# Optimization experiments

Measured on AMD Instinct MI355X. Metric: run time of the kernel, lower is better.

Reference implementation:

```python
import jax, jax.numpy as jnp
import numpy as np

EPS = 1e-5

def _layer_norm_last(x):
    # F.layer_norm over the last dim, no affine
    m = jnp.mean(x, axis=-1, keepdims=True)
    v = jnp.var(x, axis=-1, keepdims=True)
    return (x - m) * jax.lax.rsqrt(v + EPS)

def setup_inputs() -> dict:
    key = jax.random.key(0)
    ks = jax.random.split(key, 4)
    N, C, H, W = 8, 512, 32, 32
    G = 8
    x = jax.random.normal(ks[0], (N, C, H, W), dtype=jnp.float32)
    w_qkv = jax.random.normal(ks[1], (3 * C, C), dtype=jnp.float32) * 0.02
    relative = jax.random.normal(ks[2], (3, 2 * C - 1), dtype=jnp.float32)
    bn_w = jnp.ones((3 * G,), dtype=jnp.float32)
    bn_b = jnp.zeros((3 * G,), dtype=jnp.float32)
    return {
        "x": x, "w_qkv": w_qkv, "relative": relative,
        "bn_w": bn_w, "bn_b": bn_b,
        "f_qr": jnp.float32(0.1), "f_kr": jnp.float32(0.1),
        "f_sv": jnp.float32(1.0), "f_sve": jnp.float32(0.1),
        "gamma": jnp.full((1,), 0.5, dtype=jnp.float32),
    }

def reference(x, w_qkv, relative, bn_w, bn_b, f_qr, f_kr, f_sv, f_sve, gamma):
    N, C, H, W = x.shape
    HW = H * W
    G = bn_w.shape[0] // 3          # groups
    gp = HW // G                    # group_planes

    # qkv transform (1x1 conv == matmul over channels) + layernorm over spatial
    x1 = x.reshape(N, C, HW)
    x1 = jnp.einsum('oc,bci->boi', w_qkv, x1)          # (N, 3C, HW)
    x1 = _layer_norm_last(x1)

    qkv = x1.reshape(N, G, 3 * C, gp)                  # row-major, matches torch
    q = qkv[:, :, :C]                                  # (N, G, C, gp)
    k = qkv[:, :, C:2 * C]
    v = qkv[:, :, 2 * C:]

    # relative position embeddings gathered to (3, C, C)
    qi = jnp.arange(C)[None, :]
    ki = jnp.arange(C)[:, None]
    rel_idx = (ki - qi + C - 1).reshape(-1)            # (C*C,) int
    emb = relative[:, rel_idx].reshape(3, C, C)
    qE, kE, vE = emb[0], emb[1], emb[2]

    # 'bgci,icj->bgcj' with emb repeated along i collapses to sum over i then outer
    qr = jnp.einsum('bgci,cj->bgcj', q, qE) * f_qr     # (N, G, C, C)
    kr = jnp.swapaxes(jnp.einsum('bgci,cj->bgcj', k, kE), 2, 3) * f_kr
    qk = jnp.einsum('bgci,bgji->bgcj', q, k)           # (N, G, C, C)

    ss = jnp.concatenate([qk, qr, kr], axis=1)         # (N, 3G, C, C)
    # BatchNorm2d (training mode: batch stats over N, C, C axes)
    mu = jnp.mean(ss, axis=(0, 2, 3), keepdims=True)
    var = jnp.var(ss, axis=(0, 2, 3), keepdims=True)
    ss = (ss - mu) * jax.lax.rsqrt(var + EPS)
    ss = ss * bn_w.reshape(1, -1, 1, 1) + bn_b.reshape(1, -1, 1, 1)

    ss = ss.reshape(N, 3, G, C, C).sum(axis=1)         # (N, G, C, C)
    sim = jax.nn.softmax(ss, axis=3)

    sv = jnp.einsum('bgci,bgij->bgjc', sim, v) * f_sv  # (N, G, gp, C)
    # 'bgci,jci->bgjc' with vE repeated along j -> same value for every j
    sve = jnp.einsum('bgci,ci->bgc', sim, vE) * f_sve  # (N, G, C)
    sve = jnp.broadcast_to(sve[:, :, None, :], sv.shape)

    so = jnp.concatenate([sv, sve], axis=-1).reshape(N, HW * 2, C)
    so = jnp.swapaxes(_layer_norm_last(jnp.swapaxes(so, 1, 2)), 1, 2)
    out = so.reshape(N, G, gp, 2, C).sum(axis=-2).reshape(N, C, H, W)
    return gamma.reshape(()) * out + x
```

## Files before the change

kernel.cpp:

```cpp
#include <hip/hip_runtime.h>
#include <math.h>

#define DEV_INLINE __device__ __forceinline__

typedef short bf16x8 __attribute__((ext_vector_type(8)));
typedef float f32x4  __attribute__((ext_vector_type(4)));


DEV_INLINE float bf2f(short h){
  union { unsigned u; float f; } x; x.u = ((unsigned)(unsigned short)h) << 16; return x.f;
}
DEV_INLINE short f2bf(float f){
  union { float f; unsigned u; } x; x.f = f;
  unsigned r = x.u + 0x7FFF + ((x.u >> 16) & 1);
  return (short)(r >> 16);
}

template<bool MAXOP>
DEV_INLINE float block_reduce_f(float v){
  __shared__ float tmp[4];
  const int lane = threadIdx.x & 63, w = threadIdx.x >> 6;
  #pragma unroll
  for (int off = 32; off; off >>= 1){
    float o = __shfl_down(v, off);
    v = MAXOP ? fmaxf(v, o) : (v + o);
  }
  __syncthreads();
  if (lane == 0) tmp[w] = v;
  __syncthreads();
  return MAXOP ? fmaxf(fmaxf(tmp[0], tmp[1]), fmaxf(tmp[2], tmp[3]))
               : (tmp[0] + tmp[1] + tmp[2] + tmp[3]);
}

DEV_INLINE double block_reduce_d(double v){
  __shared__ double tmp[4];
  const int lane = threadIdx.x & 63, w = threadIdx.x >> 6;
  #pragma unroll
  for (int off = 32; off; off >>= 1) v += __shfl_down(v, off);
  __syncthreads();
  if (lane == 0) tmp[w] = v;
  __syncthreads();
  return tmp[0] + tmp[1] + tmp[2] + tmp[3];
}


DEV_INLINE void stage_tile(const short* __restrict__ g, int ldk, char* lds_region, int t){
  #pragma unroll
  for (int r = 0; r < 2; ++r){
    int o   = t * 16 + r * 4096;
    int row = o >> 6, wb = o & 63;
    int swb = wb ^ (((row >> 1) & 3) << 4);
    const short* src = g + (size_t)row * ldk + (swb >> 1);
    char* dst = lds_region + ((t >> 6) << 10) + (r << 12);
    __builtin_amdgcn_global_load_lds((const __attribute__((address_space(1))) void*)src,
                                     (__attribute__((address_space(3))) void*)dst, 16, 0, 0);
  }
}

DEV_INLINE bf16x8 read_frag(const char* base, int row, int kgrp){
  int off = row * 64 + ((kgrp ^ ((row >> 1) & 3)) << 4);
  return *(const bf16x8*)(base + off);
}

template<int KTILES>
DEV_INLINE void mfma_loop(const short* __restrict__ A, int ldA,
                          const short* __restrict__ B, int ldB,
                          char* ldsA, char* ldsB, int t, f32x4 acc[4][4]){
  const int l = t & 63, w = t >> 6;
  const int wr = (w >> 1) * 64, wc = (w & 1) * 64;
  for (int kt = 0; kt < KTILES; ++kt){
    stage_tile(A + kt * 32, ldA, ldsA, t);
    stage_tile(B + kt * 32, ldB, ldsB, t);
    __syncthreads();
    bf16x8 af[4], bfr[4];
    #pragma unroll
    for (int m = 0; m < 4; ++m) af[m]  = read_frag(ldsA, wr + m * 16 + (l & 15), l >> 4);
    #pragma unroll
    for (int n = 0; n < 4; ++n) bfr[n] = read_frag(ldsB, wc + n * 16 + (l & 15), l >> 4);
    #pragma unroll
    for (int m = 0; m < 4; ++m)
      #pragma unroll
      for (int n = 0; n < 4; ++n)
        acc[m][n] = __builtin_amdgcn_mfma_f32_16x16x32_bf16(af[m], bfr[n], acc[m][n], 0, 0, 0);
    __syncthreads();
  }
}

__global__ __launch_bounds__(256) void k_cvtW(const float* __restrict__ W, short* __restrict__ Wbf){
  int i = (blockIdx.x * 256 + threadIdx.x) * 4;
  float4 v = *(const float4*)(W + i);
  short4 o; o.x = f2bf(v.x); o.y = f2bf(v.y); o.z = f2bf(v.z); o.w = f2bf(v.w);
  *(short4*)(Wbf + i) = o;
}

__global__ __launch_bounds__(256) void k_cvtXt(const float* __restrict__ X, short* __restrict__ Xt){
  const int b = blockIdx.z, kt = blockIdx.y, it = blockIdx.x;
  __shared__ short s[64][72];
  const int t = threadIdx.x;
  const int rl = t >> 2, cs = (t & 3) * 16;
  const float* src = X + ((size_t)b * 512 + kt * 64 + rl) * 1024 + it * 64 + cs;
  #pragma unroll
  for (int e = 0; e < 16; e += 4){
    float4 v = *(const float4*)(src + e);
    s[rl][cs + e + 0] = f2bf(v.x); s[rl][cs + e + 1] = f2bf(v.y);
    s[rl][cs + e + 2] = f2bf(v.z); s[rl][cs + e + 3] = f2bf(v.w);
  }
  __syncthreads();
  bf16x8 a0, a1;
  #pragma unroll
  for (int e = 0; e < 8; ++e){ a0[e] = s[cs + e][rl]; a1[e] = s[cs + 8 + e][rl]; }
  short* dst = Xt + ((size_t)b * 1024 + it * 64 + rl) * 512 + kt * 64 + cs;
  *(bf16x8*)dst = a0;
  *(bf16x8*)(dst + 8) = a1;
}

__global__ __launch_bounds__(256) void k_vt(const short* __restrict__ Ybf, short* __restrict__ Vt){
  const int bg = blockIdx.z, iit = blockIdx.y, jt = blockIdx.x;
  const int b = bg >> 3, g = bg & 7;
  const short* V = Ybf + (size_t)(b * 1536 + g * 192 + 128) * 1024;
  __shared__ short s[64][72];
  const int t = threadIdx.x;
  const int rl = t >> 2, cs = (t & 3) * 16;
  const short* src = V + (size_t)(iit * 64 + rl) * 128 + jt * 64 + cs;
  *(bf16x8*)&s[rl][cs]     = *(const bf16x8*)src;
  *(bf16x8*)&s[rl][cs + 8] = *(const bf16x8*)(src + 8);
  __syncthreads();
  bf16x8 a0, a1;
  #pragma unroll
  for (int e = 0; e < 8; ++e){ a0[e] = s[cs + e][rl]; a1[e] = s[cs + 8 + e][rl]; }
  short* dst = Vt + ((size_t)bg * 128 + jt * 64 + rl) * 512 + iit * 64 + cs;
  *(bf16x8*)dst = a0;
  *(bf16x8*)(dst + 8) = a1;
}

__global__ __launch_bounds__(256) void k_gemm1(const short* __restrict__ Wbf,
                                               const short* __restrict__ Xt,
                                               short* __restrict__ Ybf){
  const int b = blockIdx.z, mt = blockIdx.y, nt = blockIdx.x;
  __shared__ char lds[16384];
  const int t = threadIdx.x;
  f32x4 acc[4][4];
  #pragma unroll
  for (int m = 0; m < 4; ++m)
    #pragma unroll
    for (int n = 0; n < 4; ++n) acc[m][n] = {0.f, 0.f, 0.f, 0.f};
  const short* A = Wbf + (size_t)mt * 128 * 512;
  const short* B = Xt + (size_t)b * 1024 * 512 + (size_t)nt * 128 * 512;
  mfma_loop<16>(A, 512, B, 512, lds, lds + 8192, t, acc);
  const int l = t & 63, w = t >> 6, wr = (w >> 1) * 64, wc = (w & 1) * 64;
  short* out = Ybf + (size_t)b * 1536 * 1024 + (size_t)(mt * 128 + wr) * 1024 + nt * 128 + wc;
  #pragma unroll
  for (int m = 0; m < 4; ++m)
    #pragma unroll
    for (int n = 0; n < 4; ++n)
      #pragma unroll
      for (int j = 0; j < 4; ++j)
        out[(size_t)(m * 16 + (l >> 4) * 4 + j) * 1024 + n * 16 + (l & 15)] = f2bf(acc[m][n][j]);
}

__global__ __launch_bounds__(256) void k_ln(short* __restrict__ Ybf,
                                            float* __restrict__ QS, float* __restrict__ KS){
  const int row = blockIdx.x * 4 + (threadIdx.x >> 6);
  const int l = threadIdx.x & 63;
  short* p = Ybf + (size_t)row * 1024 + l * 16;
  bf16x8 v0 = *(const bf16x8*)p;
  bf16x8 v1 = *(const bf16x8*)(p + 8);
  float f[16];
  #pragma unroll
  for (int e = 0; e < 8; ++e){ f[e] = bf2f(v0[e]); f[8 + e] = bf2f(v1[e]); }
  float s1 = 0.f, s2 = 0.f;
  #pragma unroll
  for (int e = 0; e < 16; ++e){ s1 += f[e]; s2 += f[e] * f[e]; }
  #pragma unroll
  for (int off = 32; off; off >>= 1){ s1 += __shfl_xor(s1, off); s2 += __shfl_xor(s2, off); }
  float mean = s1 * (1.f / 1024.f);
  float r = rsqrtf(s2 * (1.f / 1024.f) - mean * mean + 1e-5f);
  float cs = 0.f;
  #pragma unroll
  for (int e = 0; e < 16; ++e){ f[e] = (f[e] - mean) * r; cs += f[e]; }
  bf16x8 o0, o1;
  #pragma unroll
  for (int e = 0; e < 8; ++e){ o0[e] = f2bf(f[e]); o1[e] = f2bf(f[8 + e]); }
  *(bf16x8*)p = o0;
  *(bf16x8*)(p + 8) = o1;
  cs += __shfl_xor(cs, 1); cs += __shfl_xor(cs, 2); cs += __shfl_xor(cs, 4);
  const int o = row % 1536, ol = o % 192;
  if ((l & 7) == 0 && ol < 128){
    const int b = row / 1536, g = o / 192;
    const int c = (ol & 63) * 8 + (l >> 3);
    const int idx = (b * 8 + g) * 512 + c;
    if (ol < 64) QS[idx] = cs; else KS[idx] = cs;
  }
}

__global__ __launch_bounds__(256) void k_rel_rowsums(const float* __restrict__ rel,
                                                     float* __restrict__ R){
  const int c = blockIdx.x * 256 + threadIdx.x;
  float a1 = 0, a2 = 0, b1 = 0, b2 = 0;
  for (int d = 0; d < 512; ++d){
    float v0 = rel[c + d];        a1 += v0; a2 += v0*v0;
    float v1 = rel[1023 + c + d]; b1 += v1; b2 += v1*v1;
  }
  R[c] = a1; R[512 + c] = a2; R[1024 + c] = b1; R[1536 + c] = b2;
}

__global__ __launch_bounds__(256) void k_qk(const short* __restrict__ Ybf,
                                            short* __restrict__ QKbf,
                                            double* __restrict__ stats){
  const int bg = blockIdx.z, mt = blockIdx.y, nt = blockIdx.x;
  const int b = bg >> 3, g = bg & 7;
  __shared__ char lds[16384];
  const int t = threadIdx.x;
  f32x4 acc[4][4];
  #pragma unroll
  for (int m = 0; m < 4; ++m)
    #pragma unroll
    for (int n = 0; n < 4; ++n) acc[m][n] = {0.f, 0.f, 0.f, 0.f};
  const short* q  = Ybf + (size_t)(b * 1536 + g * 192) * 1024;
  const short* kp = q + 65536;
  mfma_loop<4>(q + (size_t)mt * 128 * 128, 128, kp + (size_t)nt * 128 * 128, 128,
               lds, lds + 8192, t, acc);
  const int l = t & 63, w = t >> 6, wr = (w >> 1) * 64, wc = (w & 1) * 64;
  short* out = QKbf + (size_t)bg * 512 * 512 + (size_t)(mt * 128 + wr) * 512 + nt * 128 + wc;
  float s1 = 0.f, s2 = 0.f;
  #pragma unroll
  for (int m = 0; m < 4; ++m)
    #pragma unroll
    for (int n = 0; n < 4; ++n)
      #pragma unroll
      for (int j = 0; j < 4; ++j){
        float vl = acc[m][n][j];
        s1 += vl; s2 += vl * vl;
        out[(size_t)(m * 16 + (l >> 4) * 4 + j) * 512 + n * 16 + (l & 15)] = f2bf(vl);
      }
  float S1 = block_reduce_f<false>(s1);
  float S2 = block_reduce_f<false>(s2);
  if (t == 0){
    atomicAdd(&stats[g * 6 + 0], (double)S1);
    atomicAdd(&stats[g * 6 + 1], (double)S2);
  }
}

__global__ __launch_bounds__(256) void k_qrkr_stats(const float* __restrict__ QS,
                                                    const float* __restrict__ KS,
                                                    const float* __restrict__ R,
                                                    double* __restrict__ stats){
  const int g = blockIdx.x, t = threadIdx.x;
  double sq1 = 0, sq2 = 0, sk1 = 0, sk2 = 0;
  for (int c = t; c < 512; c += 256){
    float qa = 0, qb = 0, ka = 0, kb = 0;
    for (int b = 0; b < 8; ++b){
      float v = QS[(size_t)(b * 8 + g) * 512 + c]; qa += v; qb += v * v;
      float w = KS[(size_t)(b * 8 + g) * 512 + c]; ka += w; kb += w * w;
    }
    sq1 += (double)R[c]        * qa;
    sq2 += (double)R[512 + c]  * qb;
    sk1 += (double)R[1024 + c] * ka;
    sk2 += (double)R[1536 + c] * kb;
  }
  sq1 = block_reduce_d(sq1);
  sq2 = block_reduce_d(sq2);
  sk1 = block_reduce_d(sk1);
  sk2 = block_reduce_d(sk2);
  if (t == 0){
    stats[g * 6 + 2] = sq1; stats[g * 6 + 3] = sq2;
    stats[g * 6 + 4] = sk1; stats[g * 6 + 5] = sk2;
  }
}

__global__ void k_finalize(const double* __restrict__ stats,
                           const float* __restrict__ bnw, const float* __restrict__ bnb,
                           const float* __restrict__ fqr, const float* __restrict__ fkr,
                           float* __restrict__ coefs){
  const int g = threadIdx.x;
  if (g >= 8) return;
  const double M = 2097152.0;
  double mu0  = stats[g*6+0] / M;
  double var0 = stats[g*6+1] / M - mu0*mu0;
  double A0 = (double)bnw[g] / sqrt(var0 + 1e-5);
  double fq = (double)fqr[0];
  double mu1  = fq * stats[g*6+2] / M;
  double var1 = fq*fq * stats[g*6+3] / M - mu1*mu1;
  double A1 = (double)bnw[8+g] / sqrt(var1 + 1e-5);
  double fk = (double)fkr[0];
  double mu2  = fk * stats[g*6+4] / M;
  double var2 = fk*fk * stats[g*6+5] / M - mu2*mu2;
  double A2 = (double)bnw[16+g] / sqrt(var2 + 1e-5);
  double Cg = ((double)bnb[g] - mu0*A0) + ((double)bnb[8+g] - mu1*A1) + ((double)bnb[16+g] - mu2*A2);
  coefs[g*4+0] = (float)A0;
  coefs[g*4+1] = (float)(A1 * fq);
  coefs[g*4+2] = (float)(A2 * fk);
  coefs[g*4+3] = (float)Cg;
}

__global__ __launch_bounds__(256) void k_softmax(short* __restrict__ QKbf,
    const float* __restrict__ QS, const float* __restrict__ KS,
    const float* __restrict__ rel, const float* __restrict__ coefs,
    const float* __restrict__ fsve, float* __restrict__ SVE){
  const int row = blockIdx.x * 4 + (threadIdx.x >> 6);
  const int l = threadIdx.x & 63;
  const int bg = row >> 9, c = row & 511, g = bg & 7;
  const float A0 = coefs[g*4+0], B2 = coefs[g*4+2], Cg = coefs[g*4+3];
  const float B1q = coefs[g*4+1] * QS[row];
  short* __restrict__ qkrow = QKbf + (size_t)row * 512;
  const float* __restrict__ ksrow = KS + (size_t)bg * 512;
  const int j0 = l * 8;
  bf16x8 qk8 = *(const bf16x8*)(qkrow + j0);
  float4 ks0 = *(const float4*)(ksrow + j0);
  float4 ks1 = *(const float4*)(ksrow + j0 + 4);
  float ks[8] = {ks0.x, ks0.y, ks0.z, ks0.w, ks1.x, ks1.y, ks1.z, ks1.w};
  const float* relq = rel + 511 + c - j0;
  const float* relk = rel + 1534 + j0 - c;
  float s[8];
  float m = -1e30f;
  #pragma unroll
  for (int e = 0; e < 8; ++e){
    s[e] = A0 * bf2f(qk8[e]) + B1q * relq[-e] + B2 * ks[e] * relk[e] + Cg;
    m = fmaxf(m, s[e]);
  }
  #pragma unroll
  for (int off = 32; off; off >>= 1) m = fmaxf(m, __shfl_xor(m, off));
  float sum = 0.f;
  #pragma unroll
  for (int e = 0; e < 8; ++e){ s[e] = __expf(s[e] - m); sum += s[e]; }
  #pragma unroll
  for (int off = 32; off; off >>= 1) sum += __shfl_xor(sum, off);
  const float inv = 1.0f / sum;
  const float* relv = rel + 2557 + c - j0;
  float sve = 0.f;
  bf16x8 p8;
  #pragma unroll
  for (int e = 0; e < 8; ++e){
    float p = s[e] * inv;
    p8[e] = f2bf(p);
    sve += p * relv[-e];
  }
  *(bf16x8*)(qkrow + j0) = p8;
  #pragma unroll
  for (int off = 32; off; off >>= 1) sve += __shfl_xor(sve, off);
  if (l == 0) SVE[row] = fsve[0] * sve;
}

__global__ __launch_bounds__(256) void k_sv(const short* __restrict__ Pbf,
                                            const short* __restrict__ Vt,
                                            const float* __restrict__ fsv,
                                            float* __restrict__ SV2){
  const int bg = blockIdx.z, mt = blockIdx.x;
  __shared__ char lds[16384];
  const int t = threadIdx.x;
  f32x4 acc[4][4];
  #pragma unroll
  for (int m = 0; m < 4; ++m)
    #pragma unroll
    for (int n = 0; n < 4; ++n) acc[m][n] = {0.f, 0.f, 0.f, 0.f};
  const short* A = Pbf + (size_t)bg * 512 * 512 + (size_t)mt * 128 * 512;
  const short* B = Vt  + (size_t)bg * 128 * 512;
  mfma_loop<16>(A, 512, B, 512, lds, lds + 8192, t, acc);
  const int l = t & 63, w = t >> 6, wr = (w >> 1) * 64, wc = (w & 1) * 64;
  const float fv = fsv[0];
  float* out = SV2 + (size_t)bg * 512 * 128 + (size_t)(mt * 128 + wr) * 128 + wc;
  #pragma unroll
  for (int m = 0; m < 4; ++m)
    #pragma unroll
    for (int n = 0; n < 4; ++n)
      #pragma unroll
      for (int j = 0; j < 4; ++j)
        out[(size_t)(m * 16 + (l >> 4) * 4 + j) * 128 + n * 16 + (l & 15)] = acc[m][n][j] * fv;
}

__global__ __launch_bounds__(256) void k_stats(const float* __restrict__ SV2,
    const float* __restrict__ SVE, float* __restrict__ MEAN, float* __restrict__ RSTD){
  const int bx = blockIdx.x;
  const int b = bx >> 9, c2 = bx & 511;
  const int t = threadIdx.x;
  const int g = t >> 5, j4 = (t & 31) * 4;
  const int bg = b * 8 + g;
  float4 v = *(const float4*)(SV2 + (size_t)bg * 65536 + (size_t)c2 * 128 + j4);
  float s1 = v.x + v.y + v.z + v.w;
  float s2 = v.x*v.x + v.y*v.y + v.z*v.z + v.w*v.w;
  if ((t & 31) == 0){
    float e = SVE[(size_t)bg * 512 + c2];
    s1 += 128.f * e; s2 += 128.f * e * e;
  }
  float S1 = block_reduce_f<false>(s1);
  float S2 = block_reduce_f<false>(s2);
  if (t == 0){
    float mean = S1 * (1.f / 2048.f);
    MEAN[bx] = mean;
    RSTD[bx] = rsqrtf(S2 * (1.f / 2048.f) - mean * mean + 1e-5f);
  }
}

__global__ __launch_bounds__(256) void k_out(const float* __restrict__ SV2,
    const float* __restrict__ SVE, const float* __restrict__ MEAN,
    const float* __restrict__ RSTD, const float* __restrict__ X,
    const float* __restrict__ gam, float* __restrict__ OUT){
  const int c2t = blockIdx.x, g = blockIdx.y, b = blockIdx.z;
  const int bg = b * 8 + g;
  const int c20 = c2t * 64;
  __shared__ float s[64][129];
  const int t = threadIdx.x;
  {
    const int col4 = (t & 31) * 4;
    #pragma unroll
    for (int r0 = 0; r0 < 64; r0 += 8){
      int row = r0 + (t >> 5);
      float4 v = *(const float4*)(SV2 + (size_t)bg * 65536 + (size_t)(c20 + row) * 128 + col4);
      s[row][col4] = v.x; s[row][col4+1] = v.y; s[row][col4+2] = v.z; s[row][col4+3] = v.w;
    }
  }
  __syncthreads();
  const int lane = t & 63, w = t >> 6;
  const int c2 = c20 + lane;
  const float mean = MEAN[b * 512 + c2];
  const float rs   = RSTD[b * 512 + c2];
  const float e    = SVE[(size_t)bg * 512 + c2];
  const float gm   = gam[0];
  for (int j = w; j < 128; j += 4){
    float v = s[lane][j];
    float o = (v + e - 2.f * mean) * rs;
    int chan = g * 64 + (j >> 1);
    size_t oi = ((size_t)b * 512 + chan) * 1024 + ((j & 1) << 9) + c2;
    OUT[oi] = gm * o + X[oi];
  }
}

extern "C" void kernel_launch(void* const* d_in, const int* in_sizes, int n_in,
                              void* d_out, int out_size, void* d_ws, size_t ws_size,
                              hipStream_t stream){
  const float* X    = (const float*)d_in[0];
  const float* W    = (const float*)d_in[1];
  const float* REL  = (const float*)d_in[2];
  const float* BNW  = (const float*)d_in[3];
  const float* BNB  = (const float*)d_in[4];
  const float* FQR  = (const float*)d_in[5];
  const float* FKR  = (const float*)d_in[6];
  const float* FSV  = (const float*)d_in[7];
  const float* FSVE = (const float*)d_in[8];
  const float* GAM  = (const float*)d_in[9];
  float* OUT = (float*)d_out;

  char* ws = (char*)d_ws;
  short*  Ybf   = (short*) (ws + 0ull);
  short*  QKbf  = (short*) (ws + 25165824ull);
  float*  SV2   = (float*) (ws + 58720256ull);
  short*  Wbf   = (short*) (ws + 75497472ull);
  short*  Xt    = (short*) (ws + 77070336ull);
  short*  Vt    = (short*) (ws + 85458944ull);
  float*  QS    = (float*) (ws + 93847552ull);
  float*  KS    = (float*) (ws + 93978624ull);
  float*  SVE   = (float*) (ws + 94109696ull);
  double* STATS = (double*)(ws + 94240768ull);
  float*  COEFS = (float*) (ws + 94241152ull);
  float*  R     = (float*) (ws + 94241280ull);
  float*  MEAN  = (float*) (ws + 94249472ull);
  float*  RSTD  = (float*) (ws + 94265856ull);

  hipMemsetAsync(STATS, 0, 48 * sizeof(double), stream);
  k_cvtW       <<<768,              256, 0, stream>>>(W, Wbf);
  k_cvtXt      <<<dim3(16, 8, 8),   256, 0, stream>>>(X, Xt);
  k_gemm1      <<<dim3(8, 12, 8),   256, 0, stream>>>(Wbf, Xt, Ybf);
  k_ln         <<<3072,             256, 0, stream>>>(Ybf, QS, KS);
  k_rel_rowsums<<<2,                256, 0, stream>>>(REL, R);
  k_qrkr_stats <<<8,                256, 0, stream>>>(QS, KS, R, STATS);
  k_qk         <<<dim3(4, 4, 64),   256, 0, stream>>>(Ybf, QKbf, STATS);
  k_finalize   <<<1,                64,  0, stream>>>(STATS, BNW, BNB, FQR, FKR, COEFS);
  k_vt         <<<dim3(2, 8, 64),   256, 0, stream>>>(Ybf, Vt);
  k_softmax    <<<8192,             256, 0, stream>>>(QKbf, QS, KS, REL, COEFS, FSVE, SVE);
  k_sv         <<<dim3(4, 1, 64),   256, 0, stream>>>(QKbf, Vt, FSV, SV2);
  k_stats      <<<4096,             256, 0, stream>>>(SV2, SVE, MEAN, RSTD);
  k_out        <<<dim3(8, 8, 8),    256, 0, stream>>>(SV2, SVE, MEAN, RSTD, X, GAM, OUT);
}
```

Before: 139.3 us.

## Double-buffer LDS tiles in MFMA loop and merge small stats kernels

```diff
diff --git a/kernel.cpp b/kernel.cpp
--- a/kernel.cpp
+++ b/kernel.cpp
@@ -65,28 +65,39 @@
 template<int KTILES>
 DEV_INLINE void mfma_loop(const short* __restrict__ A, int ldA,
                           const short* __restrict__ B, int ldB,
-                          char* ldsA, char* ldsB, int t, f32x4 acc[4][4]){
+                          char* lds, int t, f32x4 acc[4][4]){
   const int l = t & 63, w = t >> 6;
   const int wr = (w >> 1) * 64, wc = (w & 1) * 64;
+  stage_tile(A, ldA, lds, t);
+  stage_tile(B, ldB, lds + 8192, t);
+  __syncthreads();
+  int cur = 0;
   for (int kt = 0; kt < KTILES; ++kt){
-    stage_tile(A + kt * 32, ldA, ldsA, t);
-    stage_tile(B + kt * 32, ldB, ldsB, t);
-    __syncthreads();
+    const char* bufA = lds + cur * 16384;
+    const char* bufB = bufA + 8192;
+    if (kt + 1 < KTILES){
+      char* nxt = lds + (cur ^ 1) * 16384;
+      stage_tile(A + (kt + 1) * 32, ldA, nxt, t);
+      stage_tile(B + (kt + 1) * 32, ldB, nxt + 8192, t);
+    }
     bf16x8 af[4], bfr[4];
     #pragma unroll
-    for (int m = 0; m < 4; ++m) af[m]  = read_frag(ldsA, wr + m * 16 + (l & 15), l >> 4);
-    #pragma unroll
-    for (int n = 0; n < 4; ++n) bfr[n] = read_frag(ldsB, wc + n * 16 + (l & 15), l >> 4);
+    for (int m = 0; m < 4; ++m) af[m]  = read_frag(bufA, wr + m * 16 + (l & 15), l >> 4);
+    #pragma unroll
+    for (int n = 0; n < 4; ++n) bfr[n] = read_frag(bufB, wc + n * 16 + (l & 15), l >> 4);
     #pragma unroll
     for (int m = 0; m < 4; ++m)
       #pragma unroll
       for (int n = 0; n < 4; ++n)
         acc[m][n] = __builtin_amdgcn_mfma_f32_16x16x32_bf16(af[m], bfr[n], acc[m][n], 0, 0, 0);
     __syncthreads();
-  }
-}
-
-__global__ __launch_bounds__(256) void k_cvtW(const float* __restrict__ W, short* __restrict__ Wbf){
+    cur ^= 1;
+  }
+}
+
+__global__ __launch_bounds__(256) void k_cvtW(const float* __restrict__ W, short* __restrict__ Wbf,
+                                              double* __restrict__ stats){
+  if (blockIdx.x == 0 && threadIdx.x < 48) stats[threadIdx.x] = 0.0;
   int i = (blockIdx.x * 256 + threadIdx.x) * 4;
   float4 v = *(const float4*)(W + i);
   short4 o; o.x = f2bf(v.x); o.y = f2bf(v.y); o.z = f2bf(v.z); o.w = f2bf(v.w);
@@ -137,7 +148,7 @@
                                                const short* __restrict__ Xt,
                                                short* __restrict__ Ybf){
   const int b = blockIdx.z, mt = blockIdx.y, nt = blockIdx.x;
-  __shared__ char lds[16384];
+  __shared__ char lds[32768];
   const int t = threadIdx.x;
   f32x4 acc[4][4];
   #pragma unroll
@@ -146,7 +157,7 @@
     for (int n = 0; n < 4; ++n) acc[m][n] = {0.f, 0.f, 0.f, 0.f};
   const short* A = Wbf + (size_t)mt * 128 * 512;
   const short* B = Xt + (size_t)b * 1024 * 512 + (size_t)nt * 128 * 512;
-  mfma_loop<16>(A, 512, B, 512, lds, lds + 8192, t, acc);
+  mfma_loop<16>(A, 512, B, 512, lds, t, acc);
   const int l = t & 63, w = t >> 6, wr = (w >> 1) * 64, wc = (w & 1) * 64;
   short* out = Ybf + (size_t)b * 1536 * 1024 + (size_t)(mt * 128 + wr) * 1024 + nt * 128 + wc;
   #pragma unroll
@@ -193,23 +204,12 @@
   }
 }
 
-__global__ __launch_bounds__(256) void k_rel_rowsums(const float* __restrict__ rel,
-                                                     float* __restrict__ R){
-  const int c = blockIdx.x * 256 + threadIdx.x;
-  float a1 = 0, a2 = 0, b1 = 0, b2 = 0;
-  for (int d = 0; d < 512; ++d){
-    float v0 = rel[c + d];        a1 += v0; a2 += v0*v0;
-    float v1 = rel[1023 + c + d]; b1 += v1; b2 += v1*v1;
-  }
-  R[c] = a1; R[512 + c] = a2; R[1024 + c] = b1; R[1536 + c] = b2;
-}
-
 __global__ __launch_bounds__(256) void k_qk(const short* __restrict__ Ybf,
                                             short* __restrict__ QKbf,
                                             double* __restrict__ stats){
   const int bg = blockIdx.z, mt = blockIdx.y, nt = blockIdx.x;
   const int b = bg >> 3, g = bg & 7;
-  __shared__ char lds[16384];
+  __shared__ char lds[32768];
   const int t = threadIdx.x;
   f32x4 acc[4][4];
   #pragma unroll
@@ -219,7 +219,7 @@
   const short* q  = Ybf + (size_t)(b * 1536 + g * 192) * 1024;
   const short* kp = q + 65536;
   mfma_loop<4>(q + (size_t)mt * 128 * 128, 128, kp + (size_t)nt * 128 * 128, 128,
-               lds, lds + 8192, t, acc);
+               lds, t, acc);
   const int l = t & 63, w = t >> 6, wr = (w >> 1) * 64, wc = (w & 1) * 64;
   short* out = QKbf + (size_t)bg * 512 * 512 + (size_t)(mt * 128 + wr) * 512 + nt * 128 + wc;
   float s1 = 0.f, s2 = 0.f;
@@ -241,56 +241,56 @@
   }
 }
 
-__global__ __launch_bounds__(256) void k_qrkr_stats(const float* __restrict__ QS,
-                                                    const float* __restrict__ KS,
-                                                    const float* __restrict__ R,
-                                                    double* __restrict__ stats){
+__global__ __launch_bounds__(256) void k_coef(const float* __restrict__ QS,
+                                              const float* __restrict__ KS,
+                                              const float* __restrict__ rel,
+                                              const double* __restrict__ stats,
+                                              const float* __restrict__ bnw,
+                                              const float* __restrict__ bnb,
+                                              const float* __restrict__ fqr,
+                                              const float* __restrict__ fkr,
+                                              float* __restrict__ coefs){
   const int g = blockIdx.x, t = threadIdx.x;
   double sq1 = 0, sq2 = 0, sk1 = 0, sk2 = 0;
   for (int c = t; c < 512; c += 256){
+    float r1 = 0, r2 = 0, r3 = 0, r4 = 0;
+    for (int d = 0; d < 512; ++d){
+      float v0 = rel[c + d];        r1 += v0; r2 += v0 * v0;
+      float v1 = rel[1023 + c + d]; r3 += v1; r4 += v1 * v1;
+    }
     float qa = 0, qb = 0, ka = 0, kb = 0;
     for (int b = 0; b < 8; ++b){
       float v = QS[(size_t)(b * 8 + g) * 512 + c]; qa += v; qb += v * v;
       float w = KS[(size_t)(b * 8 + g) * 512 + c]; ka += w; kb += w * w;
     }
-    sq1 += (double)R[c]        * qa;
-    sq2 += (double)R[512 + c]  * qb;
-    sk1 += (double)R[1024 + c] * ka;
-    sk2 += (double)R[1536 + c] * kb;
+    sq1 += (double)r1 * qa;
+    sq2 += (double)r2 * qb;
+    sk1 += (double)r3 * ka;
+    sk2 += (double)r4 * kb;
   }
   sq1 = block_reduce_d(sq1);
   sq2 = block_reduce_d(sq2);
   sk1 = block_reduce_d(sk1);
   sk2 = block_reduce_d(sk2);
   if (t == 0){
-    stats[g * 6 + 2] = sq1; stats[g * 6 + 3] = sq2;
-    stats[g * 6 + 4] = sk1; stats[g * 6 + 5] = sk2;
-  }
-}
-
-__global__ void k_finalize(const double* __restrict__ stats,
-                           const float* __restrict__ bnw, const float* __restrict__ bnb,
-                           const float* __restrict__ fqr, const float* __restrict__ fkr,
-                           float* __restrict__ coefs){
-  const int g = threadIdx.x;
-  if (g >= 8) return;
-  const double M = 2097152.0;
-  double mu0  = stats[g*6+0] / M;
-  double var0 = stats[g*6+1] / M - mu0*mu0;
-  double A0 = (double)bnw[g] / sqrt(var0 + 1e-5);
-  double fq = (double)fqr[0];
-  double mu1  = fq * stats[g*6+2] / M;
-  double var1 = fq*fq * stats[g*6+3] / M - mu1*mu1;
-  double A1 = (double)bnw[8+g] / sqrt(var1 + 1e-5);
-  double fk = (double)fkr[0];
-  double mu2  = fk * stats[g*6+4] / M;
-  double var2 = fk*fk * stats[g*6+5] / M - mu2*mu2;
-  double A2 = (double)bnw[16+g] / sqrt(var2 + 1e-5);
-  double Cg = ((double)bnb[g] - mu0*A0) + ((double)bnb[8+g] - mu1*A1) + ((double)bnb[16+g] - mu2*A2);
-  coefs[g*4+0] = (float)A0;
-  coefs[g*4+1] = (float)(A1 * fq);
-  coefs[g*4+2] = (float)(A2 * fk);
-  coefs[g*4+3] = (float)Cg;
+    const double M = 2097152.0;
+    double mu0  = stats[g*6+0] / M;
+    double var0 = stats[g*6+1] / M - mu0*mu0;
+    double A0 = (double)bnw[g] / sqrt(var0 + 1e-5);
+    double fq = (double)fqr[0];
+    double mu1  = fq * sq1 / M;
+    double var1 = fq*fq * sq2 / M - mu1*mu1;
+    double A1 = (double)bnw[8+g] / sqrt(var1 + 1e-5);
+    double fk = (double)fkr[0];
+    double mu2  = fk * sk1 / M;
+    double var2 = fk*fk * sk2 / M - mu2*mu2;
+    double A2 = (double)bnw[16+g] / sqrt(var2 + 1e-5);
+    double Cg = ((double)bnb[g] - mu0*A0) + ((double)bnb[8+g] - mu1*A1) + ((double)bnb[16+g] - mu2*A2);
+    coefs[g*4+0] = (float)A0;
+    coefs[g*4+1] = (float)(A1 * fq);
+    coefs[g*4+2] = (float)(A2 * fk);
+    coefs[g*4+3] = (float)Cg;
+  }
 }
 
 __global__ __launch_bounds__(256) void k_softmax(short* __restrict__ QKbf,
@@ -346,7 +346,7 @@
                                             const float* __restrict__ fsv,
                                             float* __restrict__ SV2){
   const int bg = blockIdx.z, mt = blockIdx.x;
-  __shared__ char lds[16384];
+  __shared__ char lds[32768];
   const int t = threadIdx.x;
   f32x4 acc[4][4];
   #pragma unroll
@@ -355,7 +355,7 @@
     for (int n = 0; n < 4; ++n) acc[m][n] = {0.f, 0.f, 0.f, 0.f};
   const short* A = Pbf + (size_t)bg * 512 * 512 + (size_t)mt * 128 * 512;
   const short* B = Vt  + (size_t)bg * 128 * 512;
-  mfma_loop<16>(A, 512, B, 512, lds, lds + 8192, t, acc);
+  mfma_loop<16>(A, 512, B, 512, lds, t, acc);
   const int l = t & 63, w = t >> 6, wr = (w >> 1) * 64, wc = (w & 1) * 64;
   const float fv = fsv[0];
   float* out = SV2 + (size_t)bg * 512 * 128 + (size_t)(mt * 128 + wr) * 128 + wc;
@@ -452,22 +452,18 @@
   float*  SVE   = (float*) (ws + 94109696ull);
   double* STATS = (double*)(ws + 94240768ull);
   float*  COEFS = (float*) (ws + 94241152ull);
-  float*  R     = (float*) (ws + 94241280ull);
   float*  MEAN  = (float*) (ws + 94249472ull);
   float*  RSTD  = (float*) (ws + 94265856ull);
 
-  hipMemsetAsync(STATS, 0, 48 * sizeof(double), stream);
-  k_cvtW       <<<768,              256, 0, stream>>>(W, Wbf);
-  k_cvtXt      <<<dim3(16, 8, 8),   256, 0, stream>>>(X, Xt);
-  k_gemm1      <<<dim3(8, 12, 8),   256, 0, stream>>>(Wbf, Xt, Ybf);
-  k_ln         <<<3072,             256, 0, stream>>>(Ybf, QS, KS);
-  k_rel_rowsums<<<2,                256, 0, stream>>>(REL, R);
-  k_qrkr_stats <<<8,                256, 0, stream>>>(QS, KS, R, STATS);
-  k_qk         <<<dim3(4, 4, 64),   256, 0, stream>>>(Ybf, QKbf, STATS);
-  k_finalize   <<<1,                64,  0, stream>>>(STATS, BNW, BNB, FQR, FKR, COEFS);
-  k_vt         <<<dim3(2, 8, 64),   256, 0, stream>>>(Ybf, Vt);
-  k_softmax    <<<8192,             256, 0, stream>>>(QKbf, QS, KS, REL, COEFS, FSVE, SVE);
-  k_sv         <<<dim3(4, 1, 64),   256, 0, stream>>>(QKbf, Vt, FSV, SV2);
-  k_stats      <<<4096,             256, 0, stream>>>(SV2, SVE, MEAN, RSTD);
-  k_out        <<<dim3(8, 8, 8),    256, 0, stream>>>(SV2, SVE, MEAN, RSTD, X, GAM, OUT);
-}
+  k_cvtW   <<<768,             256, 0, stream>>>(W, Wbf, STATS);
+  k_cvtXt  <<<dim3(16, 8, 8),  256, 0, stream>>>(X, Xt);
+  k_gemm1  <<<dim3(8, 12, 8),  256, 0, stream>>>(Wbf, Xt, Ybf);
+  k_ln     <<<3072,            256, 0, stream>>>(Ybf, QS, KS);
+  k_qk     <<<dim3(4, 4, 64),  256, 0, stream>>>(Ybf, QKbf, STATS);
+  k_coef   <<<8,               256, 0, stream>>>(QS, KS, REL, STATS, BNW, BNB, FQR, FKR, COEFS);
+  k_vt     <<<dim3(2, 8, 64),  256, 0, stream>>>(Ybf, Vt);
+  k_softmax<<<8192,            256, 0, stream>>>(QKbf, QS, KS, REL, COEFS, FSVE, SVE);
+  k_sv     <<<dim3(4, 1, 64),  256, 0, stream>>>(QKbf, Vt, FSV, SV2);
+  k_stats  <<<4096,            256, 0, stream>>>(SV2, SVE, MEAN, RSTD);
+  k_out    <<<dim3(8, 8, 8),   256, 0, stream>>>(SV2, SVE, MEAN, RSTD, X, GAM, OUT);
+}
```

Measured after the change: 146.4 us. 5.1% more time.

## Fuse layernorm stats into sv epilogue and store SV in bf16

Applied to the files above, without the earlier changes.

```diff
diff --git a/kernel.cpp b/kernel.cpp
--- a/kernel.cpp
+++ b/kernel.cpp
@@ -86,8 +86,12 @@
   }
 }
 
-__global__ __launch_bounds__(256) void k_cvtW(const float* __restrict__ W, short* __restrict__ Wbf){
-  int i = (blockIdx.x * 256 + threadIdx.x) * 4;
+__global__ __launch_bounds__(256) void k_cvtW(const float* __restrict__ W, short* __restrict__ Wbf,
+                                              double* __restrict__ stats, float* __restrict__ S12){
+  const int gi = blockIdx.x * 256 + threadIdx.x;
+  if (gi < 48) stats[gi] = 0.0;
+  if (gi < 8192) S12[gi] = 0.f;
+  int i = gi * 4;
   float4 v = *(const float4*)(W + i);
   short4 o; o.x = f2bf(v.x); o.y = f2bf(v.y); o.z = f2bf(v.z); o.w = f2bf(v.w);
   *(short4*)(Wbf + i) = o;
@@ -296,7 +300,7 @@
 __global__ __launch_bounds__(256) void k_softmax(short* __restrict__ QKbf,
     const float* __restrict__ QS, const float* __restrict__ KS,
     const float* __restrict__ rel, const float* __restrict__ coefs,
-    const float* __restrict__ fsve, float* __restrict__ SVE){
+    const float* __restrict__ fsve, float* __restrict__ SVE, float* __restrict__ S12){
   const int row = blockIdx.x * 4 + (threadIdx.x >> 6);
   const int l = threadIdx.x & 63;
   const int bg = row >> 9, c = row & 511, g = bg & 7;
@@ -338,16 +342,25 @@
   *(bf16x8*)(qkrow + j0) = p8;
   #pragma unroll
   for (int off = 32; off; off >>= 1) sve += __shfl_xor(sve, off);
-  if (l == 0) SVE[row] = fsve[0] * sve;
+  if (l == 0){
+    float e = fsve[0] * sve;
+    SVE[row] = e;
+    const int b = bg >> 3;
+    atomicAdd(&S12[b * 512 + c],        128.f * e);
+    atomicAdd(&S12[4096 + b * 512 + c], 128.f * e * e);
+  }
 }
 
 __global__ __launch_bounds__(256) void k_sv(const short* __restrict__ Pbf,
                                             const short* __restrict__ Vt,
                                             const float* __restrict__ fsv,
-                                            float* __restrict__ SV2){
+                                            short* __restrict__ SV2,
+                                            float* __restrict__ S12){
   const int bg = blockIdx.z, mt = blockIdx.x;
   __shared__ char lds[16384];
-  const int t = threadIdx.x;
+  __shared__ float s1buf[128], s2buf[128];
+  const int t = threadIdx.x;
+  s1buf[t & 127] = 0.f; s2buf[t & 127] = 0.f;
   f32x4 acc[4][4];
   #pragma unroll
   for (int m = 0; m < 4; ++m)
@@ -358,62 +371,63 @@
   mfma_loop<16>(A, 512, B, 512, lds, lds + 8192, t, acc);
   const int l = t & 63, w = t >> 6, wr = (w >> 1) * 64, wc = (w & 1) * 64;
   const float fv = fsv[0];
-  float* out = SV2 + (size_t)bg * 512 * 128 + (size_t)(mt * 128 + wr) * 128 + wc;
-  #pragma unroll
-  for (int m = 0; m < 4; ++m)
-    #pragma unroll
-    for (int n = 0; n < 4; ++n)
-      #pragma unroll
-      for (int j = 0; j < 4; ++j)
-        out[(size_t)(m * 16 + (l >> 4) * 4 + j) * 128 + n * 16 + (l & 15)] = acc[m][n][j] * fv;
-}
-
-__global__ __launch_bounds__(256) void k_stats(const float* __restrict__ SV2,
-    const float* __restrict__ SVE, float* __restrict__ MEAN, float* __restrict__ RSTD){
-  const int bx = blockIdx.x;
-  const int b = bx >> 9, c2 = bx & 511;
-  const int t = threadIdx.x;
-  const int g = t >> 5, j4 = (t & 31) * 4;
-  const int bg = b * 8 + g;
-  float4 v = *(const float4*)(SV2 + (size_t)bg * 65536 + (size_t)c2 * 128 + j4);
-  float s1 = v.x + v.y + v.z + v.w;
-  float s2 = v.x*v.x + v.y*v.y + v.z*v.z + v.w*v.w;
-  if ((t & 31) == 0){
-    float e = SVE[(size_t)bg * 512 + c2];
-    s1 += 128.f * e; s2 += 128.f * e * e;
-  }
-  float S1 = block_reduce_f<false>(s1);
-  float S2 = block_reduce_f<false>(s2);
-  if (t == 0){
-    float mean = S1 * (1.f / 2048.f);
-    MEAN[bx] = mean;
-    RSTD[bx] = rsqrtf(S2 * (1.f / 2048.f) - mean * mean + 1e-5f);
-  }
-}
-
-__global__ __launch_bounds__(256) void k_out(const float* __restrict__ SV2,
-    const float* __restrict__ SVE, const float* __restrict__ MEAN,
-    const float* __restrict__ RSTD, const float* __restrict__ X,
-    const float* __restrict__ gam, float* __restrict__ OUT){
+  short* out = SV2 + (size_t)bg * 512 * 128 + (size_t)(mt * 128 + wr) * 128 + wc;
+  #pragma unroll
+  for (int m = 0; m < 4; ++m)
+    #pragma unroll
+    for (int jr = 0; jr < 4; ++jr){
+      float p1 = 0.f, p2 = 0.f;
+      #pragma unroll
+      for (int n = 0; n < 4; ++n){
+        float vl = acc[m][n][jr] * fv;
+        p1 += vl; p2 += vl * vl;
+        out[(size_t)(m * 16 + (l >> 4) * 4 + jr) * 128 + n * 16 + (l & 15)] = f2bf(vl);
+      }
+      #pragma unroll
+      for (int off = 1; off < 16; off <<= 1){
+        p1 += __shfl_xor(p1, off);
+        p2 += __shfl_xor(p2, off);
+      }
+      if ((l & 15) == 0){
+        int rloc = wr + m * 16 + (l >> 4) * 4 + jr;
+        atomicAdd(&s1buf[rloc], p1);
+        atomicAdd(&s2buf[rloc], p2);
+      }
+    }
+  __syncthreads();
+  if (t < 128){
+    const int b = bg >> 3;
+    const int ci = b * 512 + mt * 128 + t;
+    atomicAdd(&S12[ci],        s1buf[t]);
+    atomicAdd(&S12[4096 + ci], s2buf[t]);
+  }
+}
+
+__global__ __launch_bounds__(256) void k_out(const short* __restrict__ SV2,
+    const float* __restrict__ SVE, const float* __restrict__ S12,
+    const float* __restrict__ X, const float* __restrict__ gam, float* __restrict__ OUT){
   const int c2t = blockIdx.x, g = blockIdx.y, b = blockIdx.z;
   const int bg = b * 8 + g;
   const int c20 = c2t * 64;
   __shared__ float s[64][129];
   const int t = threadIdx.x;
   {
-    const int col4 = (t & 31) * 4;
-    #pragma unroll
-    for (int r0 = 0; r0 < 64; r0 += 8){
-      int row = r0 + (t >> 5);
-      float4 v = *(const float4*)(SV2 + (size_t)bg * 65536 + (size_t)(c20 + row) * 128 + col4);
-      s[row][col4] = v.x; s[row][col4+1] = v.y; s[row][col4+2] = v.z; s[row][col4+3] = v.w;
+    const int col8 = (t & 15) * 8;
+    #pragma unroll
+    for (int r0 = 0; r0 < 64; r0 += 16){
+      int row = r0 + (t >> 4);
+      bf16x8 v = *(const bf16x8*)(SV2 + (size_t)bg * 65536 + (size_t)(c20 + row) * 128 + col8);
+      #pragma unroll
+      for (int e = 0; e < 8; ++e) s[row][col8 + e] = bf2f(v[e]);
     }
   }
   __syncthreads();
   const int lane = t & 63, w = t >> 6;
   const int c2 = c20 + lane;
-  const float mean = MEAN[b * 512 + c2];
-  const float rs   = RSTD[b * 512 + c2];
+  const float sm1 = S12[b * 512 + c2];
+  const float sm2 = S12[4096 + b * 512 + c2];
+  const float mean = sm1 * (1.f / 2048.f);
+  const float rs   = rsqrtf(sm2 * (1.f / 2048.f) - mean * mean + 1e-5f);
   const float e    = SVE[(size_t)bg * 512 + c2];
   const float gm   = gam[0];
   for (int j = w; j < 128; j += 4){
@@ -443,7 +457,7 @@
   char* ws = (char*)d_ws;
   short*  Ybf   = (short*) (ws + 0ull);
   short*  QKbf  = (short*) (ws + 25165824ull);
-  float*  SV2   = (float*) (ws + 58720256ull);
+  short*  SV2   = (short*) (ws + 58720256ull);
   short*  Wbf   = (short*) (ws + 75497472ull);
   short*  Xt    = (short*) (ws + 77070336ull);
   short*  Vt    = (short*) (ws + 85458944ull);
@@ -453,21 +467,18 @@
   double* STATS = (double*)(ws + 94240768ull);
   float*  COEFS = (float*) (ws + 94241152ull);
   float*  R     = (float*) (ws + 94241280ull);
-  float*  MEAN  = (float*) (ws + 94249472ull);
-  float*  RSTD  = (float*) (ws + 94265856ull);
-
-  hipMemsetAsync(STATS, 0, 48 * sizeof(double), stream);
-  k_cvtW       <<<768,              256, 0, stream>>>(W, Wbf);
-  k_cvtXt      <<<dim3(16, 8, 8),   256, 0, stream>>>(X, Xt);
-  k_gemm1      <<<dim3(8, 12, 8),   256, 0, stream>>>(Wbf, Xt, Ybf);
-  k_ln         <<<3072,             256, 0, stream>>>(Ybf, QS, KS);
-  k_rel_rowsums<<<2,                256, 0, stream>>>(REL, R);
-  k_qrkr_stats <<<8,                256, 0, stream>>>(QS, KS, R, STATS);
-  k_qk         <<<dim3(4, 4, 64),   256, 0, stream>>>(Ybf, QKbf, STATS);
-  k_finalize   <<<1,                64,  0, stream>>>(STATS, BNW, BNB, FQR, FKR, COEFS);
-  k_vt         <<<dim3(2, 8, 64),   256, 0, stream>>>(Ybf, Vt);
-  k_softmax    <<<8192,             256, 0, stream>>>(QKbf, QS, KS, REL, COEFS, FSVE, SVE);
-  k_sv         <<<dim3(4, 1, 64),   256, 0, stream>>>(QKbf, Vt, FSV, SV2);
-  k_stats      <<<4096,             256, 0, stream>>>(SV2, SVE, MEAN, RSTD);
-  k_out        <<<dim3(8, 8, 8),    256, 0, stream>>>(SV2, SVE, MEAN, RSTD, X, GAM, OUT);
-}
+  float*  S12   = (float*) (ws + 94249472ull);
+
+  k_cvtW       <<<768,             256, 0, stream>>>(W, Wbf, STATS, S12);
+  k_cvtXt      <<<dim3(16, 8, 8),  256, 0, stream>>>(X, Xt);
+  k_gemm1      <<<dim3(8, 12, 8),  256, 0, stream>>>(Wbf, Xt, Ybf);
+  k_ln         <<<3072,            256, 0, stream>>>(Ybf, QS, KS);
+  k_rel_rowsums<<<2,               256, 0, stream>>>(REL, R);
+  k_qrkr_stats <<<8,               256, 0, stream>>>(QS, KS, R, STATS);
+  k_qk         <<<dim3(4, 4, 64),  256, 0, stream>>>(Ybf, QKbf, STATS);
+  k_finalize   <<<1,               64,  0, stream>>>(STATS, BNW, BNB, FQR, FKR, COEFS);
+  k_vt         <<<dim3(2, 8, 64),  256, 0, stream>>>(Ybf, Vt);
+  k_softmax    <<<8192,            256, 0, stream>>>(QKbf, QS, KS, REL, COEFS, FSVE, SVE, S12);
+  k_sv         <<<dim3(4, 1, 64),  256, 0, stream>>>(QKbf, Vt, FSV, SV2, S12);
+  k_out        <<<dim3(8, 8, 8),   256, 0, stream>>>(SV2, SVE, S12, X, GAM, OUT);
+}
```

Measured after the change: 136.8 us. Within noise of the previous version (-1.8%).
